# Kernel optimization log

Hardware: AMD Instinct MI355X
Metric: run time of the kernel (lower is better)

The kernel has to match this reference:

```python
import jax, jax.numpy as jnp
import numpy as np

HEADS, BS, HALO = 8, 8, 3
WIN = BS + 2 * HALO  # 14


def setup_inputs() -> dict:
    key = jax.random.key(0)
    k1, k2, k3, k4 = jax.random.split(key, 4)
    B, C, H, W = 16, 256, 64, 64
    dim_out_qk, dim_out_v = 256, 256
    std = C ** (-0.5)
    x = jax.random.normal(k1, (B, C, H, W), jnp.float32)
    Wq = jax.random.normal(k2, (dim_out_qk, C), jnp.float32) * std
    Wkv = jax.random.normal(k3, (dim_out_qk + dim_out_v, C), jnp.float32) * std
    pos_bias = jax.random.normal(k4, (HEADS, BS * BS, WIN * WIN), jnp.float32) * 0.02
    return {"x": x, "Wq": Wq, "Wkv": Wkv, "pos_bias": pos_bias}


def reference(x, Wq, Wkv, pos_bias):
    B, C, H, W = x.shape
    dhqk = Wq.shape[0] // HEADS            # 32
    dhv = Wkv.shape[0] // HEADS - dhqk     # 32
    scale = dhqk ** (-0.5)
    nhb, nwb = H // BS, W // BS
    nb = nhb * nwb

    xl = jnp.transpose(x, (0, 2, 3, 1))    # [B, H, W, C]

    # queries: [B, heads, nb, bs^2, dhqk] (row-major within block)
    q = xl @ Wq.T
    q = q.reshape(B, nhb, BS, nwb, BS, HEADS, dhqk)
    q = q.transpose(0, 5, 1, 3, 2, 4, 6).reshape(B, HEADS, nb, BS * BS, dhqk)

    # keys/values via overlapping halo windows (zero-padded unfold)
    kv = xl @ Wkv.T                                       # [B, H, W, dim_kv]
    kv = jnp.pad(kv, ((0, 0), (HALO, HALO), (HALO, HALO), (0, 0)))
    ridx = (jnp.arange(nhb) * BS)[:, None] + jnp.arange(WIN)[None, :]
    cidx = (jnp.arange(nwb) * BS)[:, None] + jnp.arange(WIN)[None, :]
    kv = kv[:, ridx]
    kv = kv[:, :, :, cidx]
    kv = kv.transpose(0, 1, 3, 2, 4, 5).reshape(B, nb, WIN * WIN, HEADS, dhqk + dhv)
    k = kv[..., :dhqk]
    v = kv[..., dhqk:]

    attn = jnp.einsum('bhnqd,bnkhd->bhnqk', q, k) * scale + pos_bias[None, :, None]
    attn = jax.nn.softmax(attn, axis=-1)
    out = jnp.einsum('bhnqk,bnkhd->bhnqd', attn, v)       # [B, heads, nb, bs^2, dhv]

    out = out.reshape(B, HEADS, nhb, nwb, BS, BS, dhv)
    out = out.transpose(0, 1, 6, 2, 4, 3, 5).reshape(B, HEADS * dhv, H, W)
    return out
```

## Files before the change

### kernel.cpp

```cpp
#include <hip/hip_runtime.h>
#include <hip/hip_bf16.h>
#include <stdint.h>

#define HEADS 8
#define WIN 14
#define NPOS 196
#define NPAD 224
#define NB 16
#define NC 256
#define NH 64
#define NW 64
#define NP 4096
#define NKV 512
#define NOC 768

typedef __bf16 bf16_t;
typedef bf16_t bf16x8 __attribute__((ext_vector_type(8)));
typedef float f32x4 __attribute__((ext_vector_type(4)));

union Frag {
  uint4 u4;
  bf16x8 b8;
  ushort us[8];
};

__device__ __forceinline__ ushort f2bf(float f) {
  bf16_t h = (bf16_t)f;
  return __builtin_bit_cast(ushort, h);
}
__device__ __forceinline__ float bf2f(ushort u) {
  uint32_t t = ((uint32_t)u) << 16;
  return __builtin_bit_cast(float, t);
}
__device__ __forceinline__ bf16x8 load_bf8(const float* __restrict__ p) {
  float4 a = *reinterpret_cast<const float4*>(p);
  float4 b = *reinterpret_cast<const float4*>(p + 4);
  bf16x8 r;
  r[0] = (bf16_t)a.x; r[1] = (bf16_t)a.y; r[2] = (bf16_t)a.z; r[3] = (bf16_t)a.w;
  r[4] = (bf16_t)b.x; r[5] = (bf16_t)b.y; r[6] = (bf16_t)b.z; r[7] = (bf16_t)b.w;
  return r;
}
__device__ __forceinline__ bf16x8 load_bf8s(const float* __restrict__ p, float s) {
  float4 a = *reinterpret_cast<const float4*>(p);
  float4 b = *reinterpret_cast<const float4*>(p + 4);
  bf16x8 r;
  r[0] = (bf16_t)(a.x * s); r[1] = (bf16_t)(a.y * s); r[2] = (bf16_t)(a.z * s); r[3] = (bf16_t)(a.w * s);
  r[4] = (bf16_t)(b.x * s); r[5] = (bf16_t)(b.y * s); r[6] = (bf16_t)(b.z * s); r[7] = (bf16_t)(b.w * s);
  return r;
}

__global__ __launch_bounds__(256) void k_wcast3(const float* __restrict__ wq,
                                                const float* __restrict__ wkv,
                                                const float* __restrict__ pb,
                                                ushort* __restrict__ wb,
                                                ushort* __restrict__ pbb) {
  const float scale = 0.17677669529663687f;
  if (blockIdx.x < 96) {
    int idx = (blockIdx.x * 256 + threadIdx.x) * 8;
    int oc = idx >> 8, c = idx & 255;
    Frag v;
    if (oc < 256) v.b8 = load_bf8s(wq + (size_t)oc * NC + c, scale);
    else          v.b8 = load_bf8(wkv + (size_t)(oc - 256) * NC + c);
    *reinterpret_cast<uint4*>(wb + idx) = v.u4;
  } else {
    int idx = ((blockIdx.x - 96) * 256 + threadIdx.x) * 8;
    Frag v;
    v.b8 = load_bf8(pb + idx);
    *reinterpret_cast<uint4*>(pbb + idx) = v.u4;
  }
}

__global__ __launch_bounds__(256, 1) void k_projF(const float* __restrict__ x,
                                                  const ushort* __restrict__ wb,
                                                  ushort* __restrict__ qkv) {
  __shared__ __align__(16) ushort As[64][264];
  const int row0 = blockIdx.x * 64;
  const int b = row0 >> 12;
  const int p0 = row0 & (NP - 1);
  const int tid = threadIdx.x, lane = tid & 63, wid = tid >> 6;
  const int quad = lane >> 4, lc = lane & 15;

  #pragma unroll
  for (int it = 0; it < 8; ++it) {
    int i = it * 256 + tid;
    int c = (i >> 4) * 2;
    int p4 = (i & 15) * 4;
    const float* src = x + ((size_t)(b * NC + c)) * NP + p0 + p4;
    float4 v0 = *reinterpret_cast<const float4*>(src);
    float4 v1 = *reinterpret_cast<const float4*>(src + NP);
    float a0[4] = {v0.x, v0.y, v0.z, v0.w};
    float a1[4] = {v1.x, v1.y, v1.z, v1.w};
    #pragma unroll
    for (int j = 0; j < 4; ++j) {
      int p = p4 + j;
      int cc = c ^ (((p >> 2) & 3) << 3);
      uint32_t pk = (uint32_t)f2bf(a0[j]) | ((uint32_t)f2bf(a1[j]) << 16);
      *reinterpret_cast<uint32_t*>(&As[p][cc]) = pk;
    }
  }
  __syncthreads();

  const int n0w = wid * 192;
  const int swz = ((lc >> 2) & 3) << 3;
  f32x4 acc[4][12] = {};
  #pragma unroll
  for (int ks = 0; ks < 8; ++ks) {
    const int k0 = ks * 32 + quad * 8;
    Frag a[4];
    #pragma unroll
    for (int mt = 0; mt < 4; ++mt)
      a[mt].u4 = *reinterpret_cast<const uint4*>(&As[mt * 16 + lc][k0 ^ swz]);
    #pragma unroll
    for (int nn = 0; nn < 12; ++nn) {
      Frag bb;
      bb.u4 = *reinterpret_cast<const uint4*>(wb + (size_t)(n0w + nn * 16 + lc) * NC + k0);
      #pragma unroll
      for (int mt = 0; mt < 4; ++mt)
        acc[mt][nn] = __builtin_amdgcn_mfma_f32_16x16x32_bf16(a[mt].b8, bb.b8, acc[mt][nn], 0, 0, 0);
    }
  }

  #pragma unroll
  for (int ch = 0; ch < 3; ++ch) {
    __syncthreads();
    #pragma unroll
    for (int nn = 0; nn < 12; ++nn) {
      int oc = n0w + nn * 16 + lc;
      if ((oc >> 8) == ch) {
        int col = oc & 255;
        #pragma unroll
        for (int mt = 0; mt < 4; ++mt)
          #pragma unroll
          for (int r = 0; r < 4; ++r)
            As[mt * 16 + quad * 4 + r][col] = f2bf(acc[mt][nn][r]);
      }
    }
    __syncthreads();
    #pragma unroll
    for (int it = 0; it < 8; ++it) {
      int i = it * 256 + tid;
      int r = i >> 5, cs = (i & 31) * 8;
      uint4 u = *reinterpret_cast<const uint4*>(&As[r][cs]);
      *reinterpret_cast<uint4*>(qkv + ((size_t)(row0 + r)) * NOC + ch * 256 + cs) = u;
    }
  }
}

__global__ __launch_bounds__(256) void k_attn_f4(const ushort* __restrict__ qkv,
                                                 const ushort* __restrict__ pbb,
                                                 float* __restrict__ out) {
  __shared__ __align__(16) ushort ksh[NPAD][40];
  __shared__ __align__(16) ushort vth[32][232];
  __shared__ __align__(16) ushort psh[4][16][32];
  float (*osh)[33] = reinterpret_cast<float(*)[33]>(&ksh[0][0]);
  const int b = blockIdx.z, h = blockIdx.y, blk = blockIdx.x;
  const int by = blk >> 3, bx = blk & 7;
  const int tid = threadIdx.x, lane = tid & 63, w = tid >> 6;
  const int quad = lane >> 4, lc = lane & 15;

  Frag aq;
  {
    int q = w * 16 + lc;
    int py = by * 8 + (q >> 3), px = bx * 8 + (q & 7);
    aq.u4 = *reinterpret_cast<const uint4*>(
        qkv + ((size_t)(b * NP + py * NW + px)) * NOC + h * 32 + quad * 8);
  }

  for (int it = 0; it < 7; ++it) {
    int i = it * 256 + tid;
    int pos = i >> 3, seg = i & 7;
    Frag v;
    v.u4 = make_uint4(0u, 0u, 0u, 0u);
    if (pos < NPOS) {
      int wy = pos / WIN;
      int wx = pos - wy * WIN;
      int yq = by * 8 - 3 + wy, xx = bx * 8 - 3 + wx;
      if ((unsigned)yq < (unsigned)NH && (unsigned)xx < (unsigned)NW)
        v.u4 = *reinterpret_cast<const uint4*>(
            qkv + ((size_t)(b * NP + yq * NW + xx)) * NOC + 256 + h * 64 + seg * 8);
    }
    if (seg < 4) {
      *reinterpret_cast<uint4*>(&ksh[pos][seg * 8]) = v.u4;
    } else {
      int d0 = (seg - 4) * 8;
      int cp = pos ^ ((seg - 4) << 3);
      #pragma unroll
      for (int j = 0; j < 8; ++j) vth[d0 + j][cp] = v.us[j];
    }
  }
  __syncthreads();

  f32x4 s[14];
  #pragma unroll
  for (int nt = 0; nt < 14; ++nt) {
    Frag bk;
    bk.u4 = *reinterpret_cast<const uint4*>(&ksh[nt * 16 + lc][quad * 8]);
    f32x4 z = {0.f, 0.f, 0.f, 0.f};
    s[nt] = __builtin_amdgcn_mfma_f32_16x16x32_bf16(aq.b8, bk.b8, z, 0, 0, 0);
  }

  const int qi = w * 16 + quad * 4;
  float lsum[4] = {0.f, 0.f, 0.f, 0.f};
  #pragma unroll
  for (int nt = 0; nt < 14; ++nt) {
    int col = nt * 16 + lc;
    #pragma unroll
    for (int r = 0; r < 4; ++r) {
      float p = 0.f;
      if (col < NPOS)
        p = __expf(s[nt][r] + bf2f(pbb[(h * 64 + qi + r) * NPOS + col]));
      s[nt][r] = p;
      lsum[r] += p;
    }
  }

  f32x4 o[2] = {};
  #pragma unroll
  for (int kt = 0; kt < 7; ++kt) {
    #pragma unroll
    for (int t = 0; t < 2; ++t)
      #pragma unroll
      for (int r = 0; r < 4; ++r)
        psh[w][quad * 4 + r][t * 16 + lc] = f2bf(s[2 * kt + t][r]);
    Frag ap;
    ap.u4 = *reinterpret_cast<const uint4*>(&psh[w][lc][quad * 8]);
    #pragma unroll
    for (int t = 0; t < 2; ++t) {
      int d = t * 16 + lc;
      int g = (kt * 4 + quad) ^ ((d >> 3) & 3);
      Frag bv;
      bv.u4 = *reinterpret_cast<const uint4*>(&vth[d][g * 8]);
      o[t] = __builtin_amdgcn_mfma_f32_16x16x32_bf16(ap.b8, bv.b8, o[t], 0, 0, 0);
    }
  }

  #pragma unroll
  for (int m = 1; m < 16; m <<= 1)
    #pragma unroll
    for (int r = 0; r < 4; ++r) lsum[r] += __shfl_xor(lsum[r], m);
  float rinv[4];
  #pragma unroll
  for (int r = 0; r < 4; ++r) rinv[r] = 1.0f / lsum[r];

  __syncthreads();
  #pragma unroll
  for (int t = 0; t < 2; ++t)
    #pragma unroll
    for (int r = 0; r < 4; ++r)
      osh[w * 16 + quad * 4 + r][t * 16 + lc] = o[t][r] * rinv[r];
  __syncthreads();

  {
    int d = tid >> 3, yy = tid & 7;
    float4 o0, o1;
    o0.x = osh[yy * 8 + 0][d]; o0.y = osh[yy * 8 + 1][d];
    o0.z = osh[yy * 8 + 2][d]; o0.w = osh[yy * 8 + 3][d];
    o1.x = osh[yy * 8 + 4][d]; o1.y = osh[yy * 8 + 5][d];
    o1.z = osh[yy * 8 + 6][d]; o1.w = osh[yy * 8 + 7][d];
    float* op = out + ((size_t)(b * NC + h * 32 + d) * NH + by * 8 + yy) * NW + bx * 8;
    *reinterpret_cast<float4*>(op) = o0;
    *reinterpret_cast<float4*>(op + 4) = o1;
  }
}

__global__ __launch_bounds__(256) void k_kv(const float* __restrict__ x,
                                            const float* __restrict__ wkv,
                                            ushort* __restrict__ kvb) {
  __shared__ __align__(16) ushort As[64][264];
  const int b = blockIdx.z;
  const int y = blockIdx.x;
  const int n0 = blockIdx.y * 128;
  const int tid = threadIdx.x;
  const int lane = tid & 63, wid = tid >> 6;
  const int quad = lane >> 4, lc = lane & 15;
  #pragma unroll
  for (int it = 0; it < 16; ++it) {
    int i = it * 256 + tid;
    int c = i >> 4, xs = (i & 15) * 4;
    float4 v = *reinterpret_cast<const float4*>(x + ((size_t)(b * NC + c)) * NP + y * NW + xs);
    As[xs + 0][c] = f2bf(v.x);
    As[xs + 1][c] = f2bf(v.y);
    As[xs + 2][c] = f2bf(v.z);
    As[xs + 3][c] = f2bf(v.w);
  }
  __syncthreads();
  const int wm = (wid & 1) * 32, wn = (wid >> 1) * 64;
  f32x4 acc[2][4] = {};
  #pragma unroll
  for (int ks = 0; ks < 8; ++ks) {
    const int k0 = ks * 32 + quad * 8;
    Frag a[2];
    bf16x8 bb[4];
    #pragma unroll
    for (int mt = 0; mt < 2; ++mt)
      a[mt].u4 = *reinterpret_cast<const uint4*>(&As[wm + mt * 16 + lc][k0]);
    #pragma unroll
    for (int nt = 0; nt < 4; ++nt) {
      int oc = n0 + wn + nt * 16 + lc;
      bb[nt] = load_bf8(wkv + (size_t)oc * NC + k0);
    }
    #pragma unroll
    for (int mt = 0; mt < 2; ++mt)
      #pragma unroll
      for (int nt = 0; nt < 4; ++nt)
        acc[mt][nt] = __builtin_amdgcn_mfma_f32_16x16x32_bf16(a[mt].b8, bb[nt], acc[mt][nt], 0, 0, 0);
  }
  #pragma unroll
  for (int mt = 0; mt < 2; ++mt) {
    #pragma unroll
    for (int r = 0; r < 4; ++r) {
      int pl = wm + mt * 16 + quad * 4 + r;
      #pragma unroll
      for (int nt = 0; nt < 4; ++nt) {
        int oc = n0 + wn + nt * 16 + lc;
        kvb[((size_t)(b * NP + y * NW + pl)) * NKV + oc] = f2bf(acc[mt][nt][r]);
      }
    }
  }
}

__global__ __launch_bounds__(256) void k_attn_v3(const float* __restrict__ x,
                                                 const float* __restrict__ wq,
                                                 const ushort* __restrict__ kvb,
                                                 const float* __restrict__ pbias,
                                                 float* __restrict__ out) {
  __shared__ __align__(16) ushort ksh[NPAD][40];
  __shared__ __align__(16) ushort vth[32][232];
  __shared__ __align__(16) ushort psh[4][16][232];
  __shared__ __align__(16) ushort qsh[4][16][32];
  __shared__ __align__(16) float osh[64][33];
  const int b = blockIdx.z, h = blockIdx.y, blk = blockIdx.x;
  const int by = blk >> 3, bx = blk & 7;
  const int tid = threadIdx.x, lane = tid & 63, w = tid >> 6;
  const int quad = lane >> 4, lc = lane & 15;

  for (int it = 0; it < 7; ++it) {
    int i = it * 256 + tid;
    int pos = i >> 3, seg = i & 7;
    Frag v;
    v.u4 = make_uint4(0u, 0u, 0u, 0u);
    if (pos < NPOS) {
      int wy = pos / WIN;
      int wx = pos - wy * WIN;
      int yq = by * 8 - 3 + wy, xx = bx * 8 - 3 + wx;
      if ((unsigned)yq < (unsigned)NH && (unsigned)xx < (unsigned)NW)
        v.u4 = *reinterpret_cast<const uint4*>(
            kvb + ((size_t)(b * NP + yq * NW + xx)) * NKV + h * 64 + seg * 8);
    }
    if (seg < 4) {
      *reinterpret_cast<uint4*>(&ksh[pos][seg * 8]) = v.u4;
    } else {
      int d0 = (seg - 4) * 8;
      #pragma unroll
      for (int j = 0; j < 8; ++j) vth[d0 + j][pos] = v.us[j];
    }
  }

  f32x4 qacc[2] = {};
  {
    const int q = w * 16 + lc;
    const size_t p = (size_t)(by * 8 + (q >> 3)) * NW + bx * 8 + (q & 7);
    #pragma unroll
    for (int ks = 0; ks < 8; ++ks) {
      const int k0 = ks * 32 + quad * 8;
      Frag ax;
      #pragma unroll
      for (int j = 0; j < 8; ++j)
        ax.us[j] = f2bf(x[((size_t)(b * NC + k0 + j)) * NP + p]);
      bf16x8 bw0 = load_bf8(wq + (size_t)(h * 32 + lc) * NC + k0);
      bf16x8 bw1 = load_bf8(wq + (size_t)(h * 32 + 16 + lc) * NC + k0);
      qacc[0] = __builtin_amdgcn_mfma_f32_16x16x32_bf16(ax.b8, bw0, qacc[0], 0, 0, 0);
      qacc[1] = __builtin_amdgcn_mfma_f32_16x16x32_bf16(ax.b8, bw1, qacc[1], 0, 0, 0);
    }
  }
  #pragma unroll
  for (int t = 0; t < 2; ++t)
    #pragma unroll
    for (int r = 0; r < 4; ++r)
      qsh[w][quad * 4 + r][t * 16 + lc] = f2bf(qacc[t][r]);
  Frag aq;
  aq.u4 = *reinterpret_cast<const uint4*>(&qsh[w][lc][quad * 8]);

  __syncthreads();

  f32x4 s[14];
  #pragma unroll
  for (int nt = 0; nt < 14; ++nt) {
    Frag bk;
    bk.u4 = *reinterpret_cast<const uint4*>(&ksh[nt * 16 + lc][quad * 8]);
    f32x4 z = {0.f, 0.f, 0.f, 0.f};
    s[nt] = __builtin_amdgcn_mfma_f32_16x16x32_bf16(aq.b8, bk.b8, z, 0, 0, 0);
  }

  const float scale = 0.17677669529663687f;
  const int qi = w * 16 + quad * 4;
  float lsum[4] = {0.f, 0.f, 0.f, 0.f};
  #pragma unroll
  for (int nt = 0; nt < 14; ++nt) {
    int col = nt * 16 + lc;
    #pragma unroll
    for (int r = 0; r < 4; ++r) {
      float p = 0.f;
      if (col < NPOS)
        p = __expf(s[nt][r] * scale + pbias[(size_t)(h * 64 + qi + r) * NPOS + col]);
      s[nt][r] = p;
      lsum[r] += p;
    }
  }
  #pragma unroll
  for (int m = 1; m < 16; m <<= 1) {
    #pragma unroll
    for (int r = 0; r < 4; ++r) lsum[r] += __shfl_xor(lsum[r], m);
  }
  #pragma unroll
  for (int nt = 0; nt < 14; ++nt) {
    #pragma unroll
    for (int r = 0; r < 4; ++r) psh[w][quad * 4 + r][nt * 16 + lc] = f2bf(s[nt][r]);
  }
  f32x4 o[2] = {};
  #pragma unroll
  for (int kt = 0; kt < 7; ++kt) {
    Frag ap;
    ap.u4 = *reinterpret_cast<const uint4*>(&psh[w][lc][kt * 32 + quad * 8]);
    #pragma unroll
    for (int t = 0; t < 2; ++t) {
      Frag bv;
      bv.u4 = *reinterpret_cast<const uint4*>(&vth[t * 16 + lc][kt * 32 + quad * 8]);
      o[t] = __builtin_amdgcn_mfma_f32_16x16x32_bf16(ap.b8, bv.b8, o[t], 0, 0, 0);
    }
  }
  #pragma unroll
  for (int t = 0; t < 2; ++t)
    #pragma unroll
    for (int r = 0; r < 4; ++r)
      osh[w * 16 + quad * 4 + r][t * 16 + lc] = o[t][r] / lsum[r];
  __syncthreads();
  {
    int d = tid >> 3, yy = tid & 7;
    float4 o0, o1;
    o0.x = osh[yy * 8 + 0][d]; o0.y = osh[yy * 8 + 1][d];
    o0.z = osh[yy * 8 + 2][d]; o0.w = osh[yy * 8 + 3][d];
    o1.x = osh[yy * 8 + 4][d]; o1.y = osh[yy * 8 + 5][d];
    o1.z = osh[yy * 8 + 6][d]; o1.w = osh[yy * 8 + 7][d];
    float* op = out + ((size_t)(b * NC + h * 32 + d) * NH + by * 8 + yy) * NW + bx * 8;
    *reinterpret_cast<float4*>(op) = o0;
    *reinterpret_cast<float4*>(op + 4) = o1;
  }
}

extern "C" void kernel_launch(void* const* d_in, const int* in_sizes, int n_in,
                              void* d_out, int out_size, void* d_ws, size_t ws_size,
                              hipStream_t stream) {
  const float* x   = (const float*)d_in[0];
  const float* wq  = (const float*)d_in[1];
  const float* wkv = (const float*)d_in[2];
  const float* pb  = (const float*)d_in[3];
  float* outp = (float*)d_out;

  const size_t qkv_elems = (size_t)NB * NP * NOC;
  const size_t wb_elems  = (size_t)NOC * NC;
  const size_t pbb_elems = (size_t)HEADS * 64 * NPOS;
  const size_t need = (qkv_elems + wb_elems + pbb_elems) * sizeof(ushort);

  if (ws_size >= need) {
    ushort* qkv = (ushort*)d_ws;
    ushort* wb  = qkv + qkv_elems;
    ushort* pbb = wb + wb_elems;
    k_wcast3<<<dim3(96 + 49), 256, 0, stream>>>(wq, wkv, pb, wb, pbb);
    k_projF<<<dim3(NB * NP / 64), 256, 0, stream>>>(x, wb, qkv);
    k_attn_f4<<<dim3(64, HEADS, NB), 256, 0, stream>>>(qkv, pbb, outp);
  } else {
    ushort* kvb = (ushort*)d_ws;
    k_kv<<<dim3(NH, NKV / 128, NB), 256, 0, stream>>>(x, wkv, kvb);
    k_attn_v3<<<dim3(64, HEADS, NB), 256, 0, stream>>>(x, wq, kvb, pb, outp);
  }
}
```

Baseline: 298.5 us.

## Split projection GEMM across output-column blocks and shrink attention LDS footprint

The projection kernel now uses a 2D grid in which each block computes one 256-column slice of the QKV output. Its accumulator drops from 48 to 16 fragments and launch bounds allow two blocks per CU, trading register pressure for more occupancy. The cost is that the x tile is loaded and converted three times. The attention kernel reuses the K shared buffer for the probability scratch and output staging, which removes a separate LDS array and moves a barrier earlier.

Result: slower. 312.7 us (+4.8%).

```diff
diff --git a/kernel.cpp b/kernel.cpp
--- a/kernel.cpp
+++ b/kernel.cpp
@@ -70,13 +70,14 @@
   }
 }
 
-__global__ __launch_bounds__(256, 1) void k_projF(const float* __restrict__ x,
+__global__ __launch_bounds__(256, 2) void k_proj3(const float* __restrict__ x,
                                                   const ushort* __restrict__ wb,
                                                   ushort* __restrict__ qkv) {
   __shared__ __align__(16) ushort As[64][264];
   const int row0 = blockIdx.x * 64;
   const int b = row0 >> 12;
   const int p0 = row0 & (NP - 1);
+  const int n0 = blockIdx.y * 256;
   const int tid = threadIdx.x, lane = tid & 63, wid = tid >> 6;
   const int quad = lane >> 4, lc = lane & 15;
 
@@ -100,59 +101,56 @@
   }
   __syncthreads();
 
-  const int n0w = wid * 192;
+  const int wm = (wid & 1) * 32, wn = (wid >> 1) * 128;
   const int swz = ((lc >> 2) & 3) << 3;
-  f32x4 acc[4][12] = {};
+  f32x4 acc[2][8] = {};
   #pragma unroll
   for (int ks = 0; ks < 8; ++ks) {
     const int k0 = ks * 32 + quad * 8;
-    Frag a[4];
-    #pragma unroll
-    for (int mt = 0; mt < 4; ++mt)
-      a[mt].u4 = *reinterpret_cast<const uint4*>(&As[mt * 16 + lc][k0 ^ swz]);
-    #pragma unroll
-    for (int nn = 0; nn < 12; ++nn) {
-      Frag bb;
-      bb.u4 = *reinterpret_cast<const uint4*>(wb + (size_t)(n0w + nn * 16 + lc) * NC + k0);
-      #pragma unroll
-      for (int mt = 0; mt < 4; ++mt)
-        acc[mt][nn] = __builtin_amdgcn_mfma_f32_16x16x32_bf16(a[mt].b8, bb.b8, acc[mt][nn], 0, 0, 0);
-    }
-  }
-
-  #pragma unroll
-  for (int ch = 0; ch < 3; ++ch) {
-    __syncthreads();
-    #pragma unroll
-    for (int nn = 0; nn < 12; ++nn) {
-      int oc = n0w + nn * 16 + lc;
-      if ((oc >> 8) == ch) {
-        int col = oc & 255;
-        #pragma unroll
-        for (int mt = 0; mt < 4; ++mt)
-          #pragma unroll
-          for (int r = 0; r < 4; ++r)
-            As[mt * 16 + quad * 4 + r][col] = f2bf(acc[mt][nn][r]);
+    Frag a0, a1;
+    a0.u4 = *reinterpret_cast<const uint4*>(&As[wm + lc][k0 ^ swz]);
+    a1.u4 = *reinterpret_cast<const uint4*>(&As[wm + 16 + lc][k0 ^ swz]);
+    #pragma unroll
+    for (int ng = 0; ng < 2; ++ng) {
+      Frag bb[4];
+      #pragma unroll
+      for (int j = 0; j < 4; ++j)
+        bb[j].u4 = *reinterpret_cast<const uint4*>(
+            wb + (size_t)(n0 + wn + (ng * 4 + j) * 16 + lc) * NC + k0);
+      #pragma unroll
+      for (int j = 0; j < 4; ++j) {
+        acc[0][ng * 4 + j] = __builtin_amdgcn_mfma_f32_16x16x32_bf16(a0.b8, bb[j].b8, acc[0][ng * 4 + j], 0, 0, 0);
+        acc[1][ng * 4 + j] = __builtin_amdgcn_mfma_f32_16x16x32_bf16(a1.b8, bb[j].b8, acc[1][ng * 4 + j], 0, 0, 0);
       }
     }
-    __syncthreads();
-    #pragma unroll
-    for (int it = 0; it < 8; ++it) {
-      int i = it * 256 + tid;
-      int r = i >> 5, cs = (i & 31) * 8;
-      uint4 u = *reinterpret_cast<const uint4*>(&As[r][cs]);
-      *reinterpret_cast<uint4*>(qkv + ((size_t)(row0 + r)) * NOC + ch * 256 + cs) = u;
-    }
-  }
-}
-
-__global__ __launch_bounds__(256) void k_attn_f4(const ushort* __restrict__ qkv,
+  }
+  __syncthreads();
+
+  #pragma unroll
+  for (int mt = 0; mt < 2; ++mt)
+    #pragma unroll
+    for (int nn = 0; nn < 8; ++nn)
+      #pragma unroll
+      for (int r = 0; r < 4; ++r)
+        As[wm + mt * 16 + quad * 4 + r][wn + nn * 16 + lc] = f2bf(acc[mt][nn][r]);
+  __syncthreads();
+  #pragma unroll
+  for (int it = 0; it < 8; ++it) {
+    int i = it * 256 + tid;
+    int r = i >> 5, cs = (i & 31) * 8;
+    uint4 u = *reinterpret_cast<const uint4*>(&As[r][cs]);
+    *reinterpret_cast<uint4*>(qkv + ((size_t)(row0 + r)) * NOC + n0 + cs) = u;
+  }
+}
+
+__global__ __launch_bounds__(256) void k_attn_f5(const ushort* __restrict__ qkv,
                                                  const ushort* __restrict__ pbb,
                                                  float* __restrict__ out) {
   __shared__ __align__(16) ushort ksh[NPAD][40];
   __shared__ __align__(16) ushort vth[32][232];
-  __shared__ __align__(16) ushort psh[4][16][32];
-  float (*osh)[33] = reinterpret_cast<float(*)[33]>(&ksh[0][0]);
+  ushort (*pshw)[32] = reinterpret_cast<ushort(*)[32]>(&ksh[0][0]);
+  float (*osh)[33] = reinterpret_cast<float(*)[33]>(
+      reinterpret_cast<char*>(&ksh[0][0]) + 4096);
   const int b = blockIdx.z, h = blockIdx.y, blk = blockIdx.x;
   const int by = blk >> 3, bx = blk & 7;
   const int tid = threadIdx.x, lane = tid & 63, w = tid >> 6;
@@ -198,6 +196,7 @@
     f32x4 z = {0.f, 0.f, 0.f, 0.f};
     s[nt] = __builtin_amdgcn_mfma_f32_16x16x32_bf16(aq.b8, bk.b8, z, 0, 0, 0);
   }
+  __syncthreads();
 
   const int qi = w * 16 + quad * 4;
   float lsum[4] = {0.f, 0.f, 0.f, 0.f};
@@ -221,9 +220,9 @@
     for (int t = 0; t < 2; ++t)
       #pragma unroll
       for (int r = 0; r < 4; ++r)
-        psh[w][quad * 4 + r][t * 16 + lc] = f2bf(s[2 * kt + t][r]);
+        pshw[w * 16 + quad * 4 + r][t * 16 + lc] = f2bf(s[2 * kt + t][r]);
     Frag ap;
-    ap.u4 = *reinterpret_cast<const uint4*>(&psh[w][lc][quad * 8]);
+    ap.u4 = *reinterpret_cast<const uint4*>(&pshw[w * 16 + lc][quad * 8]);
     #pragma unroll
     for (int t = 0; t < 2; ++t) {
       int d = t * 16 + lc;
@@ -242,7 +241,6 @@
   #pragma unroll
   for (int r = 0; r < 4; ++r) rinv[r] = 1.0f / lsum[r];
 
-  __syncthreads();
   #pragma unroll
   for (int t = 0; t < 2; ++t)
     #pragma unroll
@@ -467,8 +465,8 @@
     ushort* wb  = qkv + qkv_elems;
     ushort* pbb = wb + wb_elems;
     k_wcast3<<<dim3(96 + 49), 256, 0, stream>>>(wq, wkv, pb, wb, pbb);
-    k_projF<<<dim3(NB * NP / 64), 256, 0, stream>>>(x, wb, qkv);
-    k_attn_f4<<<dim3(64, HEADS, NB), 256, 0, stream>>>(qkv, pbb, outp);
+    k_proj3<<<dim3(NB * NP / 64, 3), 256, 0, stream>>>(x, wb, qkv);
+    k_attn_f5<<<dim3(64, HEADS, NB), 256, 0, stream>>>(qkv, pbb, outp);
   } else {
     ushort* kvb = (ushort*)d_ws;
     k_kv<<<dim3(NH, NKV / 128, NB), 256, 0, stream>>>(x, wkv, kvb);
```
